# Optimization experiments

Hardware: AMD Instinct MI355X
Metric: run time of the kernel (lower is better)

Reference implementation:

```python
import jax, jax.numpy as jnp
import numpy as np

B, S, D = 32, 200, 256          # batch, seq_len (hard-coded 200), emb_dim (hard-coded 256)
H_CLS, H_TNS, H = 2, 4, 6       # classical heads, tensor heads, total (rate=1/3, num_heads=6)
DFF, VOCAB, L, TD = 1024, 3500, 8, 2


def layer_norm(x, g, b, eps=1e-6):
    m = x.mean(-1, keepdims=True)
    v = ((x - m) ** 2).mean(-1, keepdims=True)
    return (x - m) * jax.lax.rsqrt(v + eps) * g + b


def setup_inputs() -> dict:
    key = jax.random.key(0)
    ks = jax.random.split(key, 12)
    n = jax.random.normal
    s1 = 1.0 / np.sqrt(4 + TD - 1.0)       # TNLayer RandomNormal stddev for A1/A4
    s2 = 1.0 / np.sqrt(4 + 2 * TD - 1.0)   # for A2/A3
    return {
        "tokens": jax.random.randint(ks[0], (B, S), 0, VOCAB),
        "tok_emb": n(ks[1], (VOCAB, D)) * 0.02,
        "pos_emb": n(ks[2], (S, D)) * 0.02,
        # stacked over L layers; axis 1 of size 3 is (q, k, v)
        "wqkv_w": n(ks[3], (L, 3, D, 2 * D)) * 0.05,
        "wqkv_b": jnp.zeros((L, 3, 2 * D)),
        "A1": n(ks[4], (L, 3, 4, TD, 4)) * s1,
        "A2": n(ks[5], (L, 3, 4, TD, TD, 8)) * s2,
        "A3": n(ks[6], (L, 3, 4, TD, TD, 8)) * s2,
        "A4": n(ks[7], (L, 3, 4, TD, 4)) * s1,
        "tnb": jnp.zeros((L, 3, 4 * D)),
        "out_w": n(ks[8], (L, H * D, D)) * 0.02,
        "out_b": jnp.zeros((L, D)),
        "ff1_w": n(ks[9], (L, D, DFF)) * 0.05,
        "ff1_b": jnp.zeros((L, DFF)),
        "ff2_w": n(ks[10], (L, DFF, D)) * 0.03,
        "ff2_b": jnp.zeros((L, D)),
        "ln1_g": jnp.ones((L, D)), "ln1_b": jnp.zeros((L, D)),
        "ln2_g": jnp.ones((L, D)), "ln2_b": jnp.zeros((L, D)),
    }


def bert_tensor_forward(tokens, tok_emb, pos_emb, wqkv_w, wqkv_b, A1, A2, A3, A4, tnb,
                        out_w, out_b, ff1_w, ff1_b, ff2_w, ff2_b, ln1_g, ln1_b, ln2_g, ln2_b):
    # embedding: positions array with start_index=1 is [0,1,...,199] -> pos_emb itself
    h = tok_emb[tokens] + pos_emb[None]                      # [B,S,D]
    # Attention_mask: 1.0 where token==0 (pad), broadcast over heads and query pos
    bias = (tokens == 0).astype(jnp.float32)[:, None, None, :] * (-1e9)  # [B,1,1,S]
    inv_sqrt_dk = 1.0 / jnp.sqrt(jnp.float32(D))

    def step(h, p):
        ww, wb, a1, a2, a3, a4, tb, ow, ob, f1w, f1b, f2w, f2b, g1, b1, g2, b2 = p
        # classical q/k/v heads: Dense(d_model * 2) -> [3,B,2,S,D]
        cls = jnp.einsum('bsd,xdf->xbsf', h, ww) + wb[:, None, None, :]
        cls = cls.reshape(3, B, S, H_CLS, D).transpose(0, 1, 3, 2, 4)
        # tensor-network q/k/v heads (TNLayer): MPO contraction over 4x4x4x4 split of D
        x6 = h.reshape(B, S, 4, 4, 4, 4)
        tns = jnp.einsum('bspqrt,xpmi,xqmnj,xrnok,xtol->xbsijkl', x6, a1, a2, a3, a4)
        tns = tns.reshape(3, B, S, 4 * D) + tb[:, None, None, :]
        tns = tns.reshape(3, B, S, H_TNS, D).transpose(0, 1, 3, 2, 4)  # [3,B,4,S,D]
        qkv = jnp.concatenate([cls, tns], axis=2)                      # [3,B,H,S,D]
        q, k, v = qkv[0], qkv[1], qkv[2]
        scores = jnp.einsum('bhqd,bhkd->bhqk', q, k) * inv_sqrt_dk + bias
        attn = jax.nn.softmax(scores, axis=-1)
        ctx = jnp.einsum('bhqk,bhkd->bhqd', attn, v)
        ctx = ctx.transpose(0, 2, 1, 3).reshape(B, S, H * D)           # [B,S,1536]
        out1 = layer_norm(h + ctx @ ow + ob, g1, b1)
        ffn = jax.nn.relu(out1 @ f1w + f1b) @ f2w + f2b
        return layer_norm(out1 + ffn, g2, b2), None

    xs = (wqkv_w, wqkv_b, A1, A2, A3, A4, tnb, out_w, out_b,
          ff1_w, ff1_b, ff2_w, ff2_b, ln1_g, ln1_b, ln2_g, ln2_b)
    h, _ = jax.lax.scan(step, h, xs)
    return h


def reference(tokens, tok_emb, pos_emb, wqkv_w, wqkv_b, A1, A2, A3, A4, tnb,
              out_w, out_b, ff1_w, ff1_b, ff2_w, ff2_b, ln1_g, ln1_b, ln2_g, ln2_b):
    return bert_tensor_forward(tokens, tok_emb, pos_emb, wqkv_w, wqkv_b, A1, A2, A3, A4,
                               tnb, out_w, out_b, ff1_w, ff1_b, ff2_w, ff2_b,
                               ln1_g, ln1_b, ln2_g, ln2_b)
```

## Files before the change

kernel.cpp:

```cpp
#include <hip/hip_runtime.h>
#include <hip/hip_bf16.h>

typedef __bf16 bf16x8 __attribute__((ext_vector_type(8)));
typedef float f32x4 __attribute__((ext_vector_type(4)));

#define NB 32
#define NS 200
#define SP 256
#define ND 256
#define NH 6
#define NL 8
#define NBS (NB*NS)
#define NZ (NB*NH)
#define SLAB (SP*ND)
#define PSTR 264

using bf16 = __hip_bfloat16;

enum { EPI_F32 = 0, EPI_RELU_BF = 1, EPI_QKVT = 2 };

__device__ __forceinline__ float b2f(bf16 x) { return __bfloat162float(x); }
__device__ __forceinline__ bf16 f2b(float x) { return __float2bfloat16(x); }
__device__ __forceinline__ unsigned short fbits(float x) { bf16 h = f2b(x); return *(unsigned short*)&h; }

__device__ __forceinline__ void gload16(const bf16* g, const short* l) {
    __builtin_amdgcn_global_load_lds(
        (const __attribute__((address_space(1))) unsigned int*)(unsigned long long)(g),
        (__attribute__((address_space(3))) unsigned int*)(unsigned long long)(l), 16, 0, 0);
}

template<int MODE>
__global__ __launch_bounds__(256)
void gemm_nt(const bf16* __restrict__ A, const bf16* __restrict__ Bm,
             int M, int N, int K, int Kspan, long long sOz,
             float* __restrict__ outF, bf16* __restrict__ outBf,
             const float* __restrict__ bias,
             const float* __restrict__ qkvb, const float* __restrict__ tnbp,
             bf16* __restrict__ Qb, bf16* __restrict__ Kb, bf16* __restrict__ Vb)
{
    __shared__ short Asl[2][128*32];
    __shared__ short Bsl[2][128*32];
    const int tid  = threadIdx.x;
    const int m0   = blockIdx.y * 128;
    const int n0   = blockIdx.x * 128;
    const int kbase= blockIdx.z * Kspan;
    const int lane = tid & 63, w = tid >> 6;
    const int wm   = (w >> 1) * 64, wn = (w & 1) * 64;
    const int fr   = lane & 15, kc = (lane >> 4) * 8;
    const int srow = lane >> 2, schk = (lane & 3) * 8;

    const bf16* Ag = A  + (long long)m0 * K + kbase;
    const bf16* Bg = Bm + (long long)n0 * K + kbase;

    f32x4 acc[4][4];
#pragma unroll
    for (int i = 0; i < 4; i++)
#pragma unroll
        for (int j = 0; j < 4; j++) acc[i][j] = (f32x4){0.f,0.f,0.f,0.f};

    auto stage = [&](int buf, int k0) {
        gload16(Ag + (long long)(w*32      + srow)*K + k0 + schk, &Asl[buf][(w*32     )*32]);
        gload16(Ag + (long long)(w*32 + 16 + srow)*K + k0 + schk, &Asl[buf][(w*32 + 16)*32]);
        gload16(Bg + (long long)(w*32      + srow)*K + k0 + schk, &Bsl[buf][(w*32     )*32]);
        gload16(Bg + (long long)(w*32 + 16 + srow)*K + k0 + schk, &Bsl[buf][(w*32 + 16)*32]);
    };

    const int nt = Kspan >> 5;
    stage(0, 0);
    for (int t = 0; t < nt; t++) {
        const int buf = t & 1;
        if (t + 1 < nt) {
            stage(buf ^ 1, (t + 1) * 32);
            asm volatile("s_waitcnt vmcnt(4)" ::: "memory");
        } else {
            asm volatile("s_waitcnt vmcnt(0)" ::: "memory");
        }
        __builtin_amdgcn_s_barrier();
        __builtin_amdgcn_sched_barrier(0);
        bf16x8 af[4], bfm[4];
#pragma unroll
        for (int i = 0; i < 4; i++) af[i]  = *(const bf16x8*)&Asl[buf][(wm + i*16 + fr)*32 + kc];
#pragma unroll
        for (int j = 0; j < 4; j++) bfm[j] = *(const bf16x8*)&Bsl[buf][(wn + j*16 + fr)*32 + kc];
#pragma unroll
        for (int i = 0; i < 4; i++)
#pragma unroll
            for (int j = 0; j < 4; j++)
                acc[i][j] = __builtin_amdgcn_mfma_f32_16x16x32_bf16(af[i], bfm[j], acc[i][j], 0, 0, 0);
        __builtin_amdgcn_s_barrier();
        __builtin_amdgcn_sched_barrier(0);
    }

    const int rq = (lane >> 4) * 4;
#pragma unroll
    for (int i = 0; i < 4; i++) {
        const int r0 = m0 + wm + i*16 + rq;
        int xq = 0, hdq = 0, dd0 = 0;
        float bvv[4];
        if (MODE == EPI_QKVT) {
            xq  = r0 / 1536;
            const int c1 = r0 - xq*1536;
            hdq = c1 >> 8; dd0 = c1 & 255;
#pragma unroll
            for (int rg = 0; rg < 4; rg++) {
                const int cc = c1 + rg;
                bvv[rg] = (cc < 512) ? qkvb[xq*512 + cc] : tnbp[xq*1024 + cc - 512];
            }
        }
#pragma unroll
        for (int j = 0; j < 4; j++) {
            const int c = n0 + wn + j*16 + fr;
            if (MODE == EPI_F32) {
#pragma unroll
                for (int rg = 0; rg < 4; rg++)
                    outF[(long long)blockIdx.z * sOz + (long long)(r0+rg)*N + c] = acc[i][j][rg];
            } else if (MODE == EPI_RELU_BF) {
                const float bv = bias[c];
#pragma unroll
                for (int rg = 0; rg < 4; rg++)
                    outBf[(long long)(r0+rg)*N + c] = f2b(fmaxf(acc[i][j][rg] + bv, 0.f));
            } else {
                const int bb = c / NS;
                const int ss = c - bb*NS;
                if (xq == 2) {
                    const long long base = ((long long)((bb*NH + hdq)*ND + dd0))*SP + ss;
#pragma unroll
                    for (int rg = 0; rg < 4; rg++)
                        Vb[base + (long long)rg*SP] = f2b(acc[i][j][rg] + bvv[rg]);
                } else {
                    bf16* dst = xq ? Kb : Qb;
                    ushort4 pk;
                    pk.x = fbits(acc[i][j][0] + bvv[0]);
                    pk.y = fbits(acc[i][j][1] + bvv[1]);
                    pk.z = fbits(acc[i][j][2] + bvv[2]);
                    pk.w = fbits(acc[i][j][3] + bvv[3]);
                    *(ushort4*)&dst[((long long)((bb*NH + hdq)*SP + ss))*ND + dd0] = pk;
                }
            }
        }
    }
}

__global__ __launch_bounds__(256)
void attn_fused(const bf16* __restrict__ Qb, const bf16* __restrict__ Kb,
                const bf16* __restrict__ Vtb, const int* __restrict__ tokens,
                bf16* __restrict__ ctx)
{
    __shared__ __align__(16) char smem[2*20480 + 1024 + 1024 + 64*PSTR*2];
    float* red   = (float*)(smem + 40960);
    float* maskv = (float*)(smem + 40960 + 1024);
    short* P     = (short*)(smem + 40960 + 2048);

    const int z  = blockIdx.x;
    const int b  = z / NH, h = z - b*NH;
    const int q0 = blockIdx.y * 64;
    const int tid = threadIdx.x;
    const int lane = tid & 63, w = tid >> 6;
    const int fr = lane & 15, qh = lane >> 4;
    const int kc = qh * 8;
    const int srow = lane >> 2, schk = (lane & 3) * 8;

    const bf16* Kp = Kb  + (long long)z * SLAB;
    const bf16* Qp = Qb  + (long long)z * SLAB;
    const bf16* Vp = Vtb + (long long)z * SLAB;

    {
        const int s = tid;
        float mv = -1e9f;
        if (s < NS && tokens[b*NS + s] != 0) mv = 0.f;
        maskv[s] = mv;
    }

    auto stage1 = [&](int buf, int k0) {
        short* Ks = (short*)(smem + buf*20480);
        short* Qs = (short*)(smem + buf*20480 + 16384);
#pragma unroll
        for (int r2 = 0; r2 < 4; r2++)
            gload16(Kp + (long long)(w*64 + r2*16 + srow)*ND + k0 + schk, &Ks[(w*64 + r2*16)*32]);
        gload16(Qp + (long long)(q0 + w*16 + srow)*ND + k0 + schk, &Qs[(w*16)*32]);
    };

    f32x4 acc[4][4];
#pragma unroll
    for (int i = 0; i < 4; i++)
#pragma unroll
        for (int j = 0; j < 4; j++) acc[i][j] = (f32x4){0.f,0.f,0.f,0.f};

    stage1(0, 0);
    for (int t = 0; t < 8; t++) {
        const int buf = t & 1;
        if (t + 1 < 8) {
            stage1(buf ^ 1, (t + 1) * 32);
            asm volatile("s_waitcnt vmcnt(5)" ::: "memory");
        } else {
            asm volatile("s_waitcnt vmcnt(0)" ::: "memory");
        }
        __builtin_amdgcn_s_barrier();
        __builtin_amdgcn_sched_barrier(0);
        const short* Ks = (const short*)(smem + buf*20480);
        const short* Qs = (const short*)(smem + buf*20480 + 16384);
        bf16x8 ak[4], bq[4];
#pragma unroll
        for (int i = 0; i < 4; i++) ak[i] = *(const bf16x8*)&Ks[(w*64 + i*16 + fr)*32 + kc];
#pragma unroll
        for (int j = 0; j < 4; j++) bq[j] = *(const bf16x8*)&Qs[(j*16 + fr)*32 + kc];
#pragma unroll
        for (int i = 0; i < 4; i++)
#pragma unroll
            for (int j = 0; j < 4; j++)
                acc[i][j] = __builtin_amdgcn_mfma_f32_16x16x32_bf16(ak[i], bq[j], acc[i][j], 0, 0, 0);
        __builtin_amdgcn_s_barrier();
        __builtin_amdgcn_sched_barrier(0);
    }

    float mk[4][4];
#pragma unroll
    for (int i = 0; i < 4; i++)
#pragma unroll
        for (int rg = 0; rg < 4; rg++) mk[i][rg] = maskv[w*64 + i*16 + qh*4 + rg];
#pragma unroll
    for (int i = 0; i < 4; i++)
#pragma unroll
        for (int j = 0; j < 4; j++)
#pragma unroll
            for (int rg = 0; rg < 4; rg++)
                acc[i][j][rg] = acc[i][j][rg] * 0.0625f + mk[i][rg];

    float pm[4];
#pragma unroll
    for (int j = 0; j < 4; j++) {
        float m = -3.0e38f;
#pragma unroll
        for (int i = 0; i < 4; i++)
#pragma unroll
            for (int rg = 0; rg < 4; rg++) m = fmaxf(m, acc[i][j][rg]);
        m = fmaxf(m, __shfl_xor(m, 16));
        m = fmaxf(m, __shfl_xor(m, 32));
        pm[j] = m;
    }
#pragma unroll
    for (int j = 0; j < 4; j++) red[w*64 + j*16 + fr] = pm[j];
    __syncthreads();
    float gm[4];
#pragma unroll
    for (int j = 0; j < 4; j++)
        gm[j] = fmaxf(fmaxf(red[j*16 + fr], red[64 + j*16 + fr]),
                      fmaxf(red[128 + j*16 + fr], red[192 + j*16 + fr]));
    float ps[4] = {0.f, 0.f, 0.f, 0.f};
#pragma unroll
    for (int i = 0; i < 4; i++)
#pragma unroll
        for (int j = 0; j < 4; j++)
#pragma unroll
            for (int rg = 0; rg < 4; rg++) {
                float e = __expf(acc[i][j][rg] - gm[j]);
                acc[i][j][rg] = e;
                ps[j] += e;
            }
#pragma unroll
    for (int j = 0; j < 4; j++) {
        ps[j] += __shfl_xor(ps[j], 16);
        ps[j] += __shfl_xor(ps[j], 32);
    }
    __syncthreads();
#pragma unroll
    for (int j = 0; j < 4; j++) red[w*64 + j*16 + fr] = ps[j];
    __syncthreads();
    float inv[4];
#pragma unroll
    for (int j = 0; j < 4; j++)
        inv[j] = 1.f / (red[j*16 + fr] + red[64 + j*16 + fr] + red[128 + j*16 + fr] + red[192 + j*16 + fr]);

#pragma unroll
    for (int i = 0; i < 4; i++)
#pragma unroll
        for (int j = 0; j < 4; j++) {
            ushort4 pk;
            pk.x = fbits(acc[i][j][0] * inv[j]);
            pk.y = fbits(acc[i][j][1] * inv[j]);
            pk.z = fbits(acc[i][j][2] * inv[j]);
            pk.w = fbits(acc[i][j][3] * inv[j]);
            *(ushort4*)&P[(j*16 + fr)*PSTR + w*64 + i*16 + qh*4] = pk;
        }
    __syncthreads();

    auto stage2 = [&](int buf, int s0) {
        short* Vs = (short*)(smem + buf*20480);
#pragma unroll
        for (int r2 = 0; r2 < 4; r2++)
            gload16(Vp + (long long)(w*64 + r2*16 + srow)*SP + s0 + schk, &Vs[(w*64 + r2*16)*32]);
    };

    f32x4 acc2[4][4];
#pragma unroll
    for (int i = 0; i < 4; i++)
#pragma unroll
        for (int j = 0; j < 4; j++) acc2[i][j] = (f32x4){0.f,0.f,0.f,0.f};

    stage2(0, 0);
    for (int t = 0; t < 7; t++) {
        const int buf = t & 1;
        if (t + 1 < 7) {
            stage2(buf ^ 1, (t + 1) * 32);
            asm volatile("s_waitcnt vmcnt(4)" ::: "memory");
        } else {
            asm volatile("s_waitcnt vmcnt(0)" ::: "memory");
        }
        __builtin_amdgcn_s_barrier();
        __builtin_amdgcn_sched_barrier(0);
        const short* Vs = (const short*)(smem + buf*20480);
        bf16x8 ap[4], bv[4];
#pragma unroll
        for (int i = 0; i < 4; i++) ap[i] = *(const bf16x8*)&P[(i*16 + fr)*PSTR + t*32 + kc];
#pragma unroll
        for (int j = 0; j < 4; j++) bv[j] = *(const bf16x8*)&Vs[(w*64 + j*16 + fr)*32 + kc];
#pragma unroll
        for (int i = 0; i < 4; i++)
#pragma unroll
            for (int j = 0; j < 4; j++)
                acc2[i][j] = __builtin_amdgcn_mfma_f32_16x16x32_bf16(ap[i], bv[j], acc2[i][j], 0, 0, 0);
        __builtin_amdgcn_s_barrier();
        __builtin_amdgcn_sched_barrier(0);
    }

#pragma unroll
    for (int i = 0; i < 4; i++)
#pragma unroll
        for (int j = 0; j < 4; j++)
#pragma unroll
            for (int rg = 0; rg < 4; rg++) {
                const int qg = q0 + i*16 + qh*4 + rg;
                if (qg < NS) {
                    const int d = w*64 + j*16 + fr;
                    ctx[((long long)(b*NS + qg))*1536 + h*256 + d] = f2b(acc2[i][j][rg]);
                }
            }
}

__global__ void embed_kernel(const int* __restrict__ tokens, const float* __restrict__ tok_emb,
                             const float* __restrict__ pos_emb, float* __restrict__ hf,
                             bf16* __restrict__ hbf)
{
    long long id = (long long)blockIdx.x * 256 + threadIdx.x;
    if (id >= (long long)NBS * ND) return;
    long long r = id >> 8;
    int j = id & 255;
    int tk = tokens[r];
    int s  = (int)(r % NS);
    float v = tok_emb[(long long)tk * ND + j] + pos_emb[s * ND + j];
    hf[id]  = v;
    hbf[id] = f2b(v);
}

__global__ __launch_bounds__(256)
void transpose_tile(const float* __restrict__ in, bf16* __restrict__ out,
                    int R, int C, long long inL, long long outL, int outStride)
{
    __shared__ float tl[32][33];
    const int l  = blockIdx.z;
    const int r0 = blockIdx.y * 32, c0 = blockIdx.x * 32;
    const float* ip = in + (long long)l * inL;
    bf16* op = out + (long long)l * outL;
    const int tx = threadIdx.x & 31, ty = threadIdx.x >> 5;
#pragma unroll
    for (int i = 0; i < 4; i++) {
        const int r = r0 + ty + i*8;
        tl[ty + i*8][tx] = ip[(long long)r * C + c0 + tx];
    }
    __syncthreads();
#pragma unroll
    for (int i = 0; i < 4; i++) {
        const int c = c0 + ty + i*8;
        op[(long long)c * outStride + r0 + tx] = f2b(tl[tx][ty + i*8]);
    }
}

__global__ __launch_bounds__(256)
void build_wtns(const float* __restrict__ A1, const float* __restrict__ A2,
                const float* __restrict__ A3, const float* __restrict__ A4,
                bf16* __restrict__ wcat)
{
    int lx = blockIdx.x;
    __shared__ float a1s[32], a2s[128], a3s[128], a4s[32];
    int t = threadIdx.x;
    if (t < 32)  { a1s[t] = A1[lx*32 + t]; a4s[t] = A4[lx*32 + t]; }
    if (t < 128) { a2s[t] = A2[lx*128 + t]; a3s[t] = A3[lx*128 + t]; }
    __syncthreads();
    int d = t;
    int p = d >> 6, q = (d >> 4) & 3, rr = (d >> 2) & 3, tt = d & 3;
    for (int i = 0; i < 4; i++) {
        float w1_0 = a1s[(p*2 + 0)*4 + i];
        float w1_1 = a1s[(p*2 + 1)*4 + i];
        for (int j = 0; j < 8; j++) {
            float c1_0 = w1_0 * a2s[((q*2+0)*2+0)*8 + j] + w1_1 * a2s[((q*2+1)*2+0)*8 + j];
            float c1_1 = w1_0 * a2s[((q*2+0)*2+1)*8 + j] + w1_1 * a2s[((q*2+1)*2+1)*8 + j];
            for (int kk = 0; kk < 8; kk++) {
                float c2_0 = c1_0 * a3s[((rr*2+0)*2+0)*8 + kk] + c1_1 * a3s[((rr*2+1)*2+0)*8 + kk];
                float c2_1 = c1_0 * a3s[((rr*2+0)*2+1)*8 + kk] + c1_1 * a3s[((rr*2+1)*2+1)*8 + kk];
                for (int ll = 0; ll < 4; ll++) {
                    float sv = c2_0 * a4s[(tt*2 + 0)*4 + ll] + c2_1 * a4s[(tt*2 + 1)*4 + ll];
                    int e = ((i*8 + j)*8 + kk)*4 + ll;
                    wcat[((long long)lx * 1536 + 512 + e) * 256 + d] = f2b(sv);
                }
            }
        }
    }
}

__global__ __launch_bounds__(256)
void ln_kernel(const float* __restrict__ raw0, const float* __restrict__ raw1,
               const float* __restrict__ bias, const float* __restrict__ resid,
               const float* __restrict__ g, const float* __restrict__ bb,
               float* __restrict__ outF, bf16* __restrict__ outBf)
{
    int w = threadIdx.x >> 6, lane = threadIdx.x & 63;
    long long r = (long long)blockIdx.x * 4 + w;
    long long base = r * ND;
    float x[4]; float s = 0.f;
#pragma unroll
    for (int c = 0; c < 4; c++) {
        int j = lane + 64*c;
        x[c] = resid[base + j] + raw0[base + j] + raw1[base + j] + bias[j];
        s += x[c];
    }
#pragma unroll
    for (int o = 32; o; o >>= 1) s += __shfl_xor(s, o);
    float mean = s * (1.f/256.f);
    float vs = 0.f;
#pragma unroll
    for (int c = 0; c < 4; c++) { float d = x[c] - mean; vs += d*d; }
#pragma unroll
    for (int o = 32; o; o >>= 1) vs += __shfl_xor(vs, o);
    float rs = rsqrtf(vs * (1.f/256.f) + 1e-6f);
#pragma unroll
    for (int c = 0; c < 4; c++) {
        int j = lane + 64*c;
        float y = (x[c] - mean) * rs * g[j] + bb[j];
        outF[base + j]  = y;
        outBf[base + j] = f2b(y);
    }
}

extern "C" void kernel_launch(void* const* d_in, const int* in_sizes, int n_in,
                              void* d_out, int out_size, void* d_ws, size_t ws_size,
                              hipStream_t stream)
{
    const int*   tokens  = (const int*)  d_in[0];
    const float* tok_emb = (const float*)d_in[1];
    const float* pos_emb = (const float*)d_in[2];
    const float* wqkv_w  = (const float*)d_in[3];
    const float* wqkv_b  = (const float*)d_in[4];
    const float* A1      = (const float*)d_in[5];
    const float* A2      = (const float*)d_in[6];
    const float* A3      = (const float*)d_in[7];
    const float* A4      = (const float*)d_in[8];
    const float* tnb     = (const float*)d_in[9];
    const float* out_w   = (const float*)d_in[10];
    const float* out_b   = (const float*)d_in[11];
    const float* ff1_w   = (const float*)d_in[12];
    const float* ff1_b   = (const float*)d_in[13];
    const float* ff2_w   = (const float*)d_in[14];
    const float* ff2_b   = (const float*)d_in[15];
    const float* ln1_g   = (const float*)d_in[16];
    const float* ln1_b   = (const float*)d_in[17];
    const float* ln2_g   = (const float*)d_in[18];
    const float* ln2_b   = (const float*)d_in[19];

    char* ws = (char*)d_ws;
    size_t off = 0;
    auto alloc = [&](size_t bytes) -> char* {
        char* p = ws + off;
        off += (bytes + 255) & ~(size_t)255;
        return p;
    };
    float* hf    = (float*)alloc((size_t)NBS * ND * 4);
    bf16*  hbf   = (bf16*) alloc((size_t)NBS * ND * 2);
    bf16*  wcat  = (bf16*) alloc(24ull * 1536 * 256 * 2);
    bf16*  owt   = (bf16*) alloc(8ull * 256 * 1536 * 2);
    bf16*  f1wt  = (bf16*) alloc(8ull * 1024 * 256 * 2);
    bf16*  f2wt  = (bf16*) alloc(8ull * 256 * 1024 * 2);
    bf16*  Qb    = (bf16*) alloc((size_t)NZ * SLAB * 2);
    bf16*  Kb    = (bf16*) alloc((size_t)NZ * SLAB * 2);
    bf16*  Vtb   = (bf16*) alloc((size_t)NZ * SLAB * 2);
    bf16*  ctxg  = (bf16*) alloc((size_t)NBS * 1536 * 2);
    bf16*  ffn   = (bf16*) alloc((size_t)NBS * 1024 * 2);
    float* raw   = (float*)alloc((size_t)NBS * ND * 4 * 2);
    float* out1f = (float*)alloc((size_t)NBS * ND * 4);
    bf16*  out1bf= (bf16*) alloc((size_t)NBS * ND * 2);
    if (off > ws_size) return;
    float* raw1 = raw + (size_t)NBS * ND;

    hipMemsetAsync(Qb, 0, (size_t)3 * NZ * SLAB * 2, stream);

    embed_kernel<<<NBS, 256, 0, stream>>>(tokens, tok_emb, pos_emb, hf, hbf);
    transpose_tile<<<dim3(16, 8, 24), 256, 0, stream>>>(
        wqkv_w, wcat, 256, 512, 256ll*512, 1536ll*256, 256);
    build_wtns<<<24, 256, 0, stream>>>(A1, A2, A3, A4, wcat);
    transpose_tile<<<dim3(8, 48, 8), 256, 0, stream>>>(
        out_w, owt, 1536, 256, 1536ll*256, 256ll*1536, 1536);
    transpose_tile<<<dim3(32, 8, 8), 256, 0, stream>>>(
        ff1_w, f1wt, 256, 1024, 256ll*1024, 1024ll*256, 256);
    transpose_tile<<<dim3(8, 32, 8), 256, 0, stream>>>(
        ff2_w, f2wt, 1024, 256, 1024ll*256, 256ll*1024, 1024);

    for (int l = 0; l < NL; l++) {
        const bf16* wl = wcat + (long long)l * 3 * 1536 * 256;
        gemm_nt<EPI_QKVT><<<dim3(50, 36, 1), 256, 0, stream>>>(
            wl, hbf, 4608, NBS, 256, 256, 0, nullptr, nullptr, nullptr,
            wqkv_b + l * 3 * 512, tnb + l * 3 * 1024, Qb, Kb, Vtb);
        attn_fused<<<dim3(NZ, 4), 256, 0, stream>>>(Qb, Kb, Vtb, tokens, ctxg);
        gemm_nt<EPI_F32><<<dim3(2, 50, 2), 256, 0, stream>>>(
            ctxg, owt + (long long)l * 256 * 1536, NBS, 256, 1536, 768, (long long)NBS*ND,
            raw, nullptr, nullptr, nullptr, nullptr, nullptr, nullptr, nullptr);
        ln_kernel<<<1600, 256, 0, stream>>>(raw, raw1, out_b + l * 256, hf,
                                            ln1_g + l * 256, ln1_b + l * 256, out1f, out1bf);
        gemm_nt<EPI_RELU_BF><<<dim3(8, 50, 1), 256, 0, stream>>>(
            out1bf, f1wt + (long long)l * 1024 * 256, NBS, 1024, 256, 256, 0,
            nullptr, ffn, ff1_b + l * 1024, nullptr, nullptr, nullptr, nullptr, nullptr);
        gemm_nt<EPI_F32><<<dim3(2, 50, 2), 256, 0, stream>>>(
            ffn, f2wt + (long long)l * 256 * 1024, NBS, 256, 1024, 512, (long long)NBS*ND,
            raw, nullptr, nullptr, nullptr, nullptr, nullptr, nullptr, nullptr);
        ln_kernel<<<1600, 256, 0, stream>>>(raw, raw1, ff2_b + l * 256, out1f,
                                            ln2_g + l * 256, ln2_b + l * 256,
                                            (l == NL - 1) ? (float*)d_out : hf, hbf);
    }
}
```

Measured before the change: 1.037 ms.

## Add dedicated 64x64-tile QKV GEMM with LDS-staged epilogue and swizzled LDS

Replaces the 128x128-tile QKV projection GEMM with a dedicated 64x64-tile kernel launched on a 100x72 grid, giving many more blocks. For Q and K outputs the epilogue stages results through LDS so each thread writes contiguous 16-element rows, instead of scattered 4-element stores. It also adds an XOR swizzle to the LDS layout in the QKV GEMM and in the attention kernel's K/Q/V tiles to reduce bank conflicts. The trade-off is that smaller tiles give less data reuse per block and need more global loads.

```diff
diff --git a/kernel.cpp b/kernel.cpp
--- a/kernel.cpp
+++ b/kernel.cpp
@@ -3,6 +3,7 @@
 
 typedef __bf16 bf16x8 __attribute__((ext_vector_type(8)));
 typedef float f32x4 __attribute__((ext_vector_type(4)));
+typedef int i32x4 __attribute__((ext_vector_type(4)));
 
 #define NB 32
 #define NS 200
@@ -17,7 +18,7 @@
 
 using bf16 = __hip_bfloat16;
 
-enum { EPI_F32 = 0, EPI_RELU_BF = 1, EPI_QKVT = 2 };
+enum { EPI_F32 = 0, EPI_RELU_BF = 1 };
 
 __device__ __forceinline__ float b2f(bf16 x) { return __bfloat162float(x); }
 __device__ __forceinline__ bf16 f2b(float x) { return __float2bfloat16(x); }
@@ -27,6 +28,125 @@
     __builtin_amdgcn_global_load_lds(
         (const __attribute__((address_space(1))) unsigned int*)(unsigned long long)(g),
         (__attribute__((address_space(3))) unsigned int*)(unsigned long long)(l), 16, 0, 0);
+}
+
+#define GUNIT(lane) ((((lane) & 3) ^ (((lane) >> 3) & 3)) * 8)
+#define RUNIT(kcu, fr) ((((kcu) ^ (((fr) >> 1) & 3))) * 8)
+
+__global__ __launch_bounds__(256)
+void gemm_qkv(const bf16* __restrict__ A, const bf16* __restrict__ Bm,
+              const float* __restrict__ qkvb, const float* __restrict__ tnbp,
+              bf16* __restrict__ Qb, bf16* __restrict__ Kb, bf16* __restrict__ Vb)
+{
+    __shared__ __align__(16) char smem[16384];
+    short* Asl0 = (short*)smem;
+    short* Bsl0 = (short*)(smem + 8192);
+    const int K = 256, N = NBS;
+    const int tid  = threadIdx.x;
+    const int m0   = blockIdx.y * 64;
+    const int n0   = blockIdx.x * 64;
+    const int lane = tid & 63, w = tid >> 6;
+    const int wm   = (w >> 1) * 32, wn = (w & 1) * 32;
+    const int fr   = lane & 15, kcu = lane >> 4;
+    const int srow = lane >> 2, schk = GUNIT(lane);
+
+    const bf16* Ag = A  + (long long)m0 * K;
+    const bf16* Bg = Bm + (long long)n0 * K;
+
+    f32x4 acc[2][2];
+#pragma unroll
+    for (int i = 0; i < 2; i++)
+#pragma unroll
+        for (int j = 0; j < 2; j++) acc[i][j] = (f32x4){0.f,0.f,0.f,0.f};
+
+    auto stage = [&](int buf, int k0) {
+        gload16(Ag + (long long)(w*16 + srow)*K + k0 + schk, &Asl0[buf*2048 + (w*16)*32]);
+        gload16(Bg + (long long)(w*16 + srow)*K + k0 + schk, &Bsl0[buf*2048 + (w*16)*32]);
+    };
+
+    stage(0, 0);
+    for (int t = 0; t < 8; t++) {
+        const int buf = t & 1;
+        if (t + 1 < 8) {
+            stage(buf ^ 1, (t + 1) * 32);
+            asm volatile("s_waitcnt vmcnt(2)" ::: "memory");
+        } else {
+            asm volatile("s_waitcnt vmcnt(0)" ::: "memory");
+        }
+        __builtin_amdgcn_s_barrier();
+        __builtin_amdgcn_sched_barrier(0);
+        bf16x8 af[2], bfm[2];
+#pragma unroll
+        for (int i = 0; i < 2; i++) af[i]  = *(const bf16x8*)&Asl0[buf*2048 + (wm + i*16 + fr)*32 + RUNIT(kcu, fr)];
+#pragma unroll
+        for (int j = 0; j < 2; j++) bfm[j] = *(const bf16x8*)&Bsl0[buf*2048 + (wn + j*16 + fr)*32 + RUNIT(kcu, fr)];
+#pragma unroll
+        for (int i = 0; i < 2; i++)
+#pragma unroll
+            for (int j = 0; j < 2; j++)
+                acc[i][j] = __builtin_amdgcn_mfma_f32_16x16x32_bf16(af[i], bfm[j], acc[i][j], 0, 0, 0);
+        __builtin_amdgcn_s_barrier();
+        __builtin_amdgcn_sched_barrier(0);
+    }
+
+    const int xq   = m0 / 1536;
+    const int c1_0 = m0 - xq*1536;
+    const int hdq  = c1_0 >> 8;
+    const int ddb  = c1_0 & 255;
+
+    if (xq < 2) {
+        short* T = (short*)smem;
+        __syncthreads();
+#pragma unroll
+        for (int i = 0; i < 2; i++) {
+            const int dl0 = wm + i*16 + kcu*4;
+            float bv[4];
+#pragma unroll
+            for (int rg = 0; rg < 4; rg++) {
+                const int cc = c1_0 + dl0 + rg;
+                bv[rg] = (cc < 512) ? qkvb[xq*512 + cc] : tnbp[xq*1024 + cc - 512];
+            }
+#pragma unroll
+            for (int j = 0; j < 2; j++) {
+                const int tok = wn + j*16 + fr;
+                ushort4 pk;
+                pk.x = fbits(acc[i][j][0] + bv[0]);
+                pk.y = fbits(acc[i][j][1] + bv[1]);
+                pk.z = fbits(acc[i][j][2] + bv[2]);
+                pk.w = fbits(acc[i][j][3] + bv[3]);
+                *(ushort4*)&T[tok*72 + dl0] = pk;
+            }
+        }
+        __syncthreads();
+        const int tt = tid >> 2;
+        const int dc = (tid & 3) * 16;
+        const int c  = n0 + tt;
+        const int bb = c / NS, ss = c - bb*NS;
+        bf16* dst = xq ? Kb : Qb;
+        bf16* dp  = dst + ((long long)((bb*NH + hdq)*SP + ss))*ND + ddb + dc;
+        *(i32x4*)dp       = *(const i32x4*)&T[tt*72 + dc];
+        *(i32x4*)(dp + 8) = *(const i32x4*)&T[tt*72 + dc + 8];
+    } else {
+#pragma unroll
+        for (int i = 0; i < 2; i++) {
+            const int dl0 = wm + i*16 + kcu*4;
+            float bv[4];
+#pragma unroll
+            for (int rg = 0; rg < 4; rg++) {
+                const int cc = c1_0 + dl0 + rg;
+                bv[rg] = (cc < 512) ? qkvb[2*512 + cc] : tnbp[2*1024 + cc - 512];
+            }
+#pragma unroll
+            for (int j = 0; j < 2; j++) {
+                const int c = n0 + wn + j*16 + fr;
+                const int bb = c / NS, ss = c - bb*NS;
+                const long long base = ((long long)((bb*NH + hdq)*ND + ddb + dl0))*SP + ss;
+#pragma unroll
+                for (int rg = 0; rg < 4; rg++)
+                    Vb[base + (long long)rg*SP] = f2b(acc[i][j][rg] + bv[rg]);
+            }
+        }
+    }
 }
 
 template<int MODE>
@@ -34,9 +154,7 @@
 void gemm_nt(const bf16* __restrict__ A, const bf16* __restrict__ Bm,
              int M, int N, int K, int Kspan, long long sOz,
              float* __restrict__ outF, bf16* __restrict__ outBf,
-             const float* __restrict__ bias,
-             const float* __restrict__ qkvb, const float* __restrict__ tnbp,
-             bf16* __restrict__ Qb, bf16* __restrict__ Kb, bf16* __restrict__ Vb)
+             const float* __restrict__ bias)
 {
     __shared__ short Asl[2][128*32];
     __shared__ short Bsl[2][128*32];
@@ -95,18 +213,6 @@
 #pragma unroll
     for (int i = 0; i < 4; i++) {
         const int r0 = m0 + wm + i*16 + rq;
-        int xq = 0, hdq = 0, dd0 = 0;
-        float bvv[4];
-        if (MODE == EPI_QKVT) {
-            xq  = r0 / 1536;
-            const int c1 = r0 - xq*1536;
-            hdq = c1 >> 8; dd0 = c1 & 255;
-#pragma unroll
-            for (int rg = 0; rg < 4; rg++) {
-                const int cc = c1 + rg;
-                bvv[rg] = (cc < 512) ? qkvb[xq*512 + cc] : tnbp[xq*1024 + cc - 512];
-            }
-        }
 #pragma unroll
         for (int j = 0; j < 4; j++) {
             const int c = n0 + wn + j*16 + fr;
@@ -114,28 +220,11 @@
 #pragma unroll
                 for (int rg = 0; rg < 4; rg++)
                     outF[(long long)blockIdx.z * sOz + (long long)(r0+rg)*N + c] = acc[i][j][rg];
-            } else if (MODE == EPI_RELU_BF) {
+            } else {
                 const float bv = bias[c];
 #pragma unroll
                 for (int rg = 0; rg < 4; rg++)
                     outBf[(long long)(r0+rg)*N + c] = f2b(fmaxf(acc[i][j][rg] + bv, 0.f));
-            } else {
-                const int bb = c / NS;
-                const int ss = c - bb*NS;
-                if (xq == 2) {
-                    const long long base = ((long long)((bb*NH + hdq)*ND + dd0))*SP + ss;
-#pragma unroll
-                    for (int rg = 0; rg < 4; rg++)
-                        Vb[base + (long long)rg*SP] = f2b(acc[i][j][rg] + bvv[rg]);
-                } else {
-                    bf16* dst = xq ? Kb : Qb;
-                    ushort4 pk;
-                    pk.x = fbits(acc[i][j][0] + bvv[0]);
-                    pk.y = fbits(acc[i][j][1] + bvv[1]);
-                    pk.z = fbits(acc[i][j][2] + bvv[2]);
-                    pk.w = fbits(acc[i][j][3] + bvv[3]);
-                    *(ushort4*)&dst[((long long)((bb*NH + hdq)*SP + ss))*ND + dd0] = pk;
-                }
             }
         }
     }
@@ -158,7 +247,7 @@
     const int lane = tid & 63, w = tid >> 6;
     const int fr = lane & 15, qh = lane >> 4;
     const int kc = qh * 8;
-    const int srow = lane >> 2, schk = (lane & 3) * 8;
+    const int srow = lane >> 2, schk = GUNIT(lane);
 
     const bf16* Kp = Kb  + (long long)z * SLAB;
     const bf16* Qp = Qb  + (long long)z * SLAB;
@@ -201,9 +290,9 @@
         const short* Qs = (const short*)(smem + buf*20480 + 16384);
         bf16x8 ak[4], bq[4];
 #pragma unroll
-        for (int i = 0; i < 4; i++) ak[i] = *(const bf16x8*)&Ks[(w*64 + i*16 + fr)*32 + kc];
-#pragma unroll
-        for (int j = 0; j < 4; j++) bq[j] = *(const bf16x8*)&Qs[(j*16 + fr)*32 + kc];
+        for (int i = 0; i < 4; i++) ak[i] = *(const bf16x8*)&Ks[(w*64 + i*16 + fr)*32 + RUNIT(qh, fr)];
+#pragma unroll
+        for (int j = 0; j < 4; j++) bq[j] = *(const bf16x8*)&Qs[(j*16 + fr)*32 + RUNIT(qh, fr)];
 #pragma unroll
         for (int i = 0; i < 4; i++)
 #pragma unroll
@@ -313,7 +402,7 @@
 #pragma unroll
         for (int i = 0; i < 4; i++) ap[i] = *(const bf16x8*)&P[(i*16 + fr)*PSTR + t*32 + kc];
 #pragma unroll
-        for (int j = 0; j < 4; j++) bv[j] = *(const bf16x8*)&Vs[(w*64 + j*16 + fr)*32 + kc];
+        for (int j = 0; j < 4; j++) bv[j] = *(const bf16x8*)&Vs[(w*64 + j*16 + fr)*32 + RUNIT(qh, fr)];
 #pragma unroll
         for (int i = 0; i < 4; i++)
 #pragma unroll
@@ -505,21 +594,20 @@
 
     for (int l = 0; l < NL; l++) {
         const bf16* wl = wcat + (long long)l * 3 * 1536 * 256;
-        gemm_nt<EPI_QKVT><<<dim3(50, 36, 1), 256, 0, stream>>>(
-            wl, hbf, 4608, NBS, 256, 256, 0, nullptr, nullptr, nullptr,
-            wqkv_b + l * 3 * 512, tnb + l * 3 * 1024, Qb, Kb, Vtb);
+        gemm_qkv<<<dim3(100, 72, 1), 256, 0, stream>>>(
+            wl, hbf, wqkv_b + l * 3 * 512, tnb + l * 3 * 1024, Qb, Kb, Vtb);
         attn_fused<<<dim3(NZ, 4), 256, 0, stream>>>(Qb, Kb, Vtb, tokens, ctxg);
         gemm_nt<EPI_F32><<<dim3(2, 50, 2), 256, 0, stream>>>(
             ctxg, owt + (long long)l * 256 * 1536, NBS, 256, 1536, 768, (long long)NBS*ND,
-            raw, nullptr, nullptr, nullptr, nullptr, nullptr, nullptr, nullptr);
+            raw, nullptr, nullptr);
         ln_kernel<<<1600, 256, 0, stream>>>(raw, raw1, out_b + l * 256, hf,
                                             ln1_g + l * 256, ln1_b + l * 256, out1f, out1bf);
         gemm_nt<EPI_RELU_BF><<<dim3(8, 50, 1), 256, 0, stream>>>(
             out1bf, f1wt + (long long)l * 1024 * 256, NBS, 1024, 256, 256, 0,
-            nullptr, ffn, ff1_b + l * 1024, nullptr, nullptr, nullptr, nullptr, nullptr);
+            nullptr, ffn, ff1_b + l * 1024);
         gemm_nt<EPI_F32><<<dim3(2, 50, 2), 256, 0, stream>>>(
             ffn, f2wt + (long long)l * 256 * 1024, NBS, 256, 1024, 512, (long long)NBS*ND,
-            raw, nullptr, nullptr, nullptr, nullptr, nullptr, nullptr, nullptr);
+            raw, nullptr, nullptr);
         ln_kernel<<<1600, 256, 0, stream>>>(raw, raw1, ff2_b + l * 256, out1f,
                                             ln2_g + l * 256, ln2_b + l * 256,
                                             (l == NL - 1) ? (float*)d_out : hf, hbf);
```

New measurement: 978.6 us. -5.6%, faster.
